# Kernel optimization log

Measured on AMD Instinct MI355X. Metric: run time of the kernel, lower is better.

The kernel has to match this reference:

```python
import jax, jax.numpy as jnp
import numpy as np

jax.config.update("jax_enable_x64", True)

# config
B, S = 4, 4096
H_SIZE = 2048          # hidden_size
VOCAB = 128000         # engram_base_vocab_size
MAX_NGRAM = 3          # engram_max_ngram_size -> orders 2..3
PRIME = 500009         # engram_n_embed_per_ngram (same prime for every order)
N_HEAD = 4             # engram_n_head_per_ngram
E = 32                 # engram_embed_dim
KS = 4                 # short conv kernel size
NUM_ORDERS = MAX_NGRAM - 1
TOTAL_HEADS = NUM_ORDERS * N_HEAD
TOTAL_ROWS = PRIME * N_HEAD * NUM_ORDERS  # flat multi-head table rows


def setup_inputs() -> dict:
    key = jax.random.key(0)
    k_ids, k_h, k_tab, k_cw, k_hp, k_gp, k_op = jax.random.split(key, 7)
    input_ids = jax.random.randint(k_ids, (B, S), 0, VOCAB, dtype=jnp.int64)
    hidden_states = jax.random.normal(k_h, (B, S, H_SIZE), dtype=jnp.float32)
    # identity compressed-tokenizer mapping buffer
    mapping = jnp.arange(VOCAB, dtype=jnp.int64)
    # deterministic odd multipliers, seeded like _build_multipliers
    rng = np.random.default_rng(0 * 10007 + 0 * 1009)
    mults = rng.integers(1, 2 ** 31, size=(NUM_ORDERS, N_HEAD, MAX_NGRAM))
    multipliers = jnp.asarray(mults * 2 + 1, dtype=jnp.int64)
    table = 0.02 * jax.random.normal(k_tab, (TOTAL_ROWS, E), dtype=jnp.float32)
    conv_w = 0.1 * jax.random.normal(k_cw, (E, KS), dtype=jnp.float32)  # depthwise taps
    conv_b = jnp.zeros((E,), dtype=jnp.float32)
    Wh = 0.05 * jax.random.normal(k_hp, (E, TOTAL_HEADS * E), dtype=jnp.float32)
    Wg = 0.02 * jax.random.normal(k_gp, (E, H_SIZE), dtype=jnp.float32)
    Wo = 0.02 * jax.random.normal(k_op, (H_SIZE, E), dtype=jnp.float32)
    return {"input_ids": input_ids, "hidden_states": hidden_states,
            "mapping": mapping, "multipliers": multipliers, "table": table,
            "conv_w": conv_w, "conv_b": conv_b, "Wh": Wh, "Wg": Wg, "Wo": Wo}


def _hash_indices(compressed, multipliers):
    """XOR-mix n-gram hash indices -> [B, S, TOTAL_HEADS] int64."""
    all_idx = []
    offset = 0
    for oi, k in enumerate(range(2, MAX_NGRAM + 1)):
        # forward sliding window, clamped at last token (matches cat/expand trick)
        pos = jnp.minimum(jnp.arange(S)[:, None] + jnp.arange(k)[None, :], S - 1)  # [S,k]
        ng = compressed[:, pos]                                  # [B,S,k]
        m = multipliers[oi, :, :k]                               # [nh,k]
        prod = ng[:, :, None, :] * m[None, None, :, :]           # [B,S,nh,k]
        h = prod[..., 0]
        for p in range(1, k):
            h = h ^ prod[..., p]
        idx = h % PRIME + (offset + jnp.arange(N_HEAD, dtype=jnp.int64) * PRIME)
        all_idx.append(idx)
        offset += PRIME * N_HEAD
    return jnp.concatenate(all_idx, axis=-1)


def reference(input_ids, hidden_states, mapping, multipliers, table,
              conv_w, conv_b, Wh, Wg, Wo):
    compressed = mapping[input_ids]                              # [B,S]
    indices = _hash_indices(compressed, multipliers)             # [B,S,TOTAL_HEADS]
    emb = table[indices].reshape(B, S, TOTAL_HEADS * E)          # multi-head gather
    emb = emb @ Wh.T                                             # head_proj -> [B,S,E]
    # causal depthwise short conv (kernel KS, left pad KS-1)
    xp = jnp.pad(emb, ((0, 0), (KS - 1, 0), (0, 0)))
    emb = sum(xp[:, j:j + S, :] * conv_w[:, j] for j in range(KS)) + conv_b
    gate = jax.nn.sigmoid(hidden_states @ Wg.T)                  # [B,S,E]
    return (gate * emb) @ Wo.T                                   # [B,S,H_SIZE]
```

## Files before the change

kernel.cpp:

```cpp
#include <hip/hip_runtime.h>
#include <hip/hip_bf16.h>
#include <stdint.h>

#define HSZ 2048
#define PRIME 500009u
#define CHUNK 64
#define NCH 32
#define WAVE_REG 16384
#define IDXOFF 65536
#define A_OFF 0
#define E36_OFF 19008
#define GE_OFF 24192

typedef __attribute__((ext_vector_type(8))) short short8;
typedef __attribute__((ext_vector_type(4))) float f32x4;
typedef __attribute__((ext_vector_type(4))) unsigned uint4v;
typedef __attribute__((ext_vector_type(2))) unsigned uint2v;

#define MEMFENCE asm volatile("" ::: "memory")
#define BARRIER() do { MEMFENCE; __builtin_amdgcn_s_barrier(); MEMFENCE; } while (0)
#define WAIT_LGKM0 asm volatile("s_waitcnt lgkmcnt(0)" ::: "memory")
#define WAIT_VM(n) asm volatile("s_waitcnt vmcnt(" #n ")" ::: "memory")

__device__ __forceinline__ unsigned pk2(float x, float y) {
  __hip_bfloat162 h = __float22bfloat162_rn(make_float2(x, y));
  return *reinterpret_cast<unsigned*>(&h);
}
__device__ __forceinline__ short f2bf(float f) {
  __hip_bfloat16 h = __float2bfloat16(f);
  return *reinterpret_cast<short*>(&h);
}
__device__ __forceinline__ short8 pack8(float4 a, float4 b) {
  uint4v u = {pk2(a.x, a.y), pk2(a.z, a.w), pk2(b.x, b.y), pk2(b.z, b.w)};
  return __builtin_bit_cast(short8, u);
}
__device__ __forceinline__ short8 load8_bf(const float* __restrict__ p) {
  float4 a = *reinterpret_cast<const float4*>(p);
  float4 b = *reinterpret_cast<const float4*>(p + 4);
  return pack8(a, b);
}
__device__ __forceinline__ void gload_lds16(const float* g, void* l) {
  __builtin_amdgcn_global_load_lds(
      (const __attribute__((address_space(1))) void*)g,
      (__attribute__((address_space(3))) void*)l, 16, 0, 0);
}

__global__ __launch_bounds__(256, 2) void engram_fused(
    const int* __restrict__ ids, const int* __restrict__ mapping,
    const unsigned* __restrict__ mult, const float* __restrict__ table,
    const float* __restrict__ Wh, const float* __restrict__ hidden,
    const float* __restrict__ cw, const float* __restrict__ cb,
    const float* __restrict__ Wg, const float* __restrict__ Wo,
    float* __restrict__ out) {
  __shared__ __align__(16) char smem[IDXOFF + 1152];
  int* idx_lds = (int*)(smem + IDXOFF);
  short(*A_lds)[264] = (short(*)[264])(smem + A_OFF);
  float(*emb36)[36] = (float(*)[36])(smem + E36_OFF);
  short(*ge_lds)[40] = (short(*)[40])(smem + GE_OFF);

  const int tid = threadIdx.x;
  const int wid = tid >> 6, lane = tid & 63;
  const int l16 = lane & 15, q = lane >> 4;
  const int t0 = blockIdx.x * 32;
  const int tt = wid >> 1, ee = wid & 1;

  char* wavebase = smem + wid * WAVE_REG;

  auto STAGE = [&](int kc) {
    char* hb = wavebase + (kc & 1) * 8192;
#pragma unroll
    for (int j = 0; j < 4; ++j) {
      int r = j * 4 + q;
      unsigned c4 = (((unsigned)l16 * 16u) ^ (((unsigned)r & 7u) << 4)) >> 2;
      gload_lds16(hidden + (size_t)(t0 + tt * 16 + r) * HSZ + kc * CHUNK + c4,
                  hb + j * 1024);
    }
#pragma unroll
    for (int j = 0; j < 4; ++j) {
      int r = j * 4 + q;
      unsigned c4 = (((unsigned)l16 * 16u) ^ (((unsigned)r & 7u) << 4)) >> 2;
      gload_lds16(Wg + (size_t)(ee * 16 + r) * HSZ + kc * CHUNK + c4,
                  hb + 4096 + j * 1024);
    }
  };

#pragma unroll
  for (int p = 0; p < 2; ++p) {
    int hh = p * 256 + tid;
    if (hh < 288) {
      int slot = hh >> 3, head = hh & 7;
      int tg = t0 - 4 + slot;
      if (tg < 0) tg = 0;
      int b = tg >> 12, s = tg & 4095;
      const int* idb = ids + (b << 12);
      int s1 = s + 1 > 4095 ? 4095 : s + 1;
      int s2 = s + 2 > 4095 ? 4095 : s + 2;
      uint64_t c0 = (unsigned)mapping[idb[s]];
      uint64_t c1 = (unsigned)mapping[idb[s1]];
      uint64_t c2 = (unsigned)mapping[idb[s2]];
      int mb = head * 3;
      uint64_t h = (c0 * (uint64_t)mult[mb]) ^ (c1 * (uint64_t)mult[mb + 1]);
      if (head >= 4) h ^= c2 * (uint64_t)mult[mb + 2];
      idx_lds[hh] = (int)((unsigned)(h % PRIME) + (unsigned)head * PRIME);
    }
  }
  WAIT_LGKM0; BARRIER();

  float4 g[9];
#pragma unroll
  for (int p = 0; p < 9; ++p) {
    int task = p * 256 + tid;
    int r = task >> 3, c4 = (task & 7) * 4;
    int row = idx_lds[r];
    g[p] = *reinterpret_cast<const float4*>(table + (size_t)row * 32 + c4);
  }

  STAGE(0);
  STAGE(1);

  const unsigned swz = ((unsigned)l16 & 7u) << 4;
  const char* hrow = wavebase + l16 * 256;
  const char* wrow = wavebase + 4096 + l16 * 256;
  const unsigned x0 = q * 32u;
  f32x4 acc = {0.f, 0.f, 0.f, 0.f};

  auto MLP_ITER = [&](int kc, bool stage_next) {
    const char* hb = hrow + (kc & 1) * 8192;
    const char* wb = wrow + (kc & 1) * 8192;
    float4 a0 = *reinterpret_cast<const float4*>(hb + (x0 ^ swz));
    float4 a1 = *reinterpret_cast<const float4*>(hb + ((x0 + 16) ^ swz));
    float4 a2 = *reinterpret_cast<const float4*>(hb + ((x0 + 128) ^ swz));
    float4 a3 = *reinterpret_cast<const float4*>(hb + ((x0 + 144) ^ swz));
    float4 b0 = *reinterpret_cast<const float4*>(wb + (x0 ^ swz));
    float4 b1 = *reinterpret_cast<const float4*>(wb + ((x0 + 16) ^ swz));
    float4 b2 = *reinterpret_cast<const float4*>(wb + ((x0 + 128) ^ swz));
    float4 b3 = *reinterpret_cast<const float4*>(wb + ((x0 + 144) ^ swz));
    short8 A0 = pack8(a0, a1), A1 = pack8(a2, a3);
    short8 B0 = pack8(b0, b1), B1 = pack8(b2, b3);
    WAIT_LGKM0;
    if (stage_next) STAGE(kc + 2);
    acc = __builtin_amdgcn_mfma_f32_16x16x32_bf16(A0, B0, acc, 0, 0, 0);
    acc = __builtin_amdgcn_mfma_f32_16x16x32_bf16(A1, B1, acc, 0, 0, 0);
  };

  for (int kc = 0; kc < NCH - 1; ++kc) {
    WAIT_VM(8);
    MLP_ITER(kc, kc < NCH - 2);
  }
  { WAIT_VM(0); MLP_ITER(NCH - 1, false); }

  BARRIER();
#pragma unroll
  for (int p = 0; p < 9; ++p) {
    int task = p * 256 + tid;
    int r = task >> 3, c4 = (task & 7) * 4;
    uint2v pk = {pk2(g[p].x, g[p].y), pk2(g[p].z, g[p].w)};
    *reinterpret_cast<uint2v*>(&A_lds[r >> 3][(r & 7) * 32 + c4]) = pk;
  }
  WAIT_LGKM0; BARRIER();

  for (int job = wid; job < 6; job += 4) {
    int jt = job >> 1;
    int base = (jt == 0) ? 0 : (jt == 1) ? 16 : 20;
    int e0 = (job & 1) * 16;
    f32x4 ac = {0.f, 0.f, 0.f, 0.f};
#pragma unroll
    for (int ks = 0; ks < 8; ++ks) {
      short8 wf = load8_bf(Wh + (size_t)(e0 + l16) * 256 + ks * 32 + q * 8);
      short8 a = *reinterpret_cast<const short8*>(&A_lds[base + l16][ks * 32 + q * 8]);
      ac = __builtin_amdgcn_mfma_f32_16x16x32_bf16(wf, a, ac, 0, 0, 0);
    }
    if (jt != 2 || l16 >= 12)
      *reinterpret_cast<f32x4*>(&emb36[base + l16][e0 + q * 4]) = ac;
  }
  WAIT_LGKM0; BARRIER();

  {
    int c = ee * 16 + l16;
    float4 cwv = *reinterpret_cast<const float4*>(cw + c * 4);
    float cbv = cb[c];
#pragma unroll
    for (int j = 0; j < 4; ++j) {
      int r = tt * 16 + q * 4 + j;
      int s = (t0 & 4095) + r;
      float v = cbv;
#pragma unroll
      for (int j2 = 0; j2 < 4; ++j2)
        if (s - 3 + j2 >= 0) v += cwv[j2] * emb36[r + 1 + j2][c];
      float gt = 1.f / (1.f + __expf(-acc[j]));
      ge_lds[r][c] = f2bf(gt * v);
    }
  }
  WAIT_LGKM0; BARRIER();

  short8 Af0 = *reinterpret_cast<const short8*>(&ge_lds[l16][q * 8]);
  short8 Af1 = *reinterpret_cast<const short8*>(&ge_lds[16 + l16][q * 8]);
  float* orow0 = out + (size_t)(t0 + l16) * HSZ;
  float* orow1 = out + (size_t)(t0 + 16 + l16) * HSZ;
  int hbase = wid * 512;
#pragma unroll 4
  for (int ht = 0; ht < 32; ++ht) {
    int h0 = hbase + ht * 16;
    short8 aw = load8_bf(Wo + (size_t)(h0 + l16) * 32 + q * 8);
    f32x4 z = {0.f, 0.f, 0.f, 0.f};
    f32x4 o0 = __builtin_amdgcn_mfma_f32_16x16x32_bf16(aw, Af0, z, 0, 0, 0);
    f32x4 o1 = __builtin_amdgcn_mfma_f32_16x16x32_bf16(aw, Af1, z, 0, 0, 0);
    *reinterpret_cast<f32x4*>(orow0 + h0 + q * 4) = o0;
    *reinterpret_cast<f32x4*>(orow1 + h0 + q * 4) = o1;
  }
}

extern "C" void kernel_launch(void* const* d_in, const int* in_sizes, int n_in,
                              void* d_out, int out_size, void* d_ws, size_t ws_size,
                              hipStream_t stream) {
  const int* ids = (const int*)d_in[0];
  const float* hidden = (const float*)d_in[1];
  const int* mapping = (const int*)d_in[2];
  const unsigned* mult = (const unsigned*)d_in[3];
  const float* table = (const float*)d_in[4];
  const float* cw = (const float*)d_in[5];
  const float* cb = (const float*)d_in[6];
  const float* Wh = (const float*)d_in[7];
  const float* Wg = (const float*)d_in[8];
  const float* Wo = (const float*)d_in[9];
  float* out = (float*)d_out;

  engram_fused<<<512, 256, 0, stream>>>(ids, mapping, mult, table, Wh, hidden,
                                        cw, cb, Wg, Wo, out);
}
```

Baseline: 74.93 us.

## Halve tokens per block and split gate K-reduction across waves

Each block now handles 16 tokens instead of 32, and the four waves split the gate GEMM's K dimension in half (two K-halves by two E-halves), with the partial sums combined through LDS. This halves LDS use per block and doubles the grid to 1024 blocks with launch bounds raised to 4 blocks per SM. The aim is more occupancy and more memory parallelism for the hidden-state streaming. In exchange there is a cross-wave reduction, more halo recomputation of hash and gather per token, and smaller MFMA work per wave in the output projection.

```diff
diff --git a/kernel.cpp b/kernel.cpp
--- a/kernel.cpp
+++ b/kernel.cpp
@@ -4,13 +4,14 @@
 
 #define HSZ 2048
 #define PRIME 500009u
-#define CHUNK 64
+#define CHUNK 32
 #define NCH 32
-#define WAVE_REG 16384
-#define IDXOFF 65536
+#define WAVE_REG 8192
+#define IDXOFF 32768
 #define A_OFF 0
-#define E36_OFF 19008
-#define GE_OFF 24192
+#define E20_OFF 10560
+#define GE_OFF 13440
+#define RED_OFF 14720
 
 typedef __attribute__((ext_vector_type(8))) short short8;
 typedef __attribute__((ext_vector_type(4))) float f32x4;
@@ -45,70 +46,67 @@
       (__attribute__((address_space(3))) void*)l, 16, 0, 0);
 }
 
-__global__ __launch_bounds__(256, 2) void engram_fused(
+__global__ __launch_bounds__(256, 4) void engram_fused(
     const int* __restrict__ ids, const int* __restrict__ mapping,
     const unsigned* __restrict__ mult, const float* __restrict__ table,
     const float* __restrict__ Wh, const float* __restrict__ hidden,
     const float* __restrict__ cw, const float* __restrict__ cb,
     const float* __restrict__ Wg, const float* __restrict__ Wo,
     float* __restrict__ out) {
-  __shared__ __align__(16) char smem[IDXOFF + 1152];
+  __shared__ __align__(16) char smem[IDXOFF + 640];
   int* idx_lds = (int*)(smem + IDXOFF);
   short(*A_lds)[264] = (short(*)[264])(smem + A_OFF);
-  float(*emb36)[36] = (float(*)[36])(smem + E36_OFF);
+  float(*emb20)[36] = (float(*)[36])(smem + E20_OFF);
   short(*ge_lds)[40] = (short(*)[40])(smem + GE_OFF);
+  float(*accred)[4][64] = (float(*)[4][64])(smem + RED_OFF);
 
   const int tid = threadIdx.x;
   const int wid = tid >> 6, lane = tid & 63;
   const int l16 = lane & 15, q = lane >> 4;
-  const int t0 = blockIdx.x * 32;
-  const int tt = wid >> 1, ee = wid & 1;
+  const int t0 = blockIdx.x * 16;
+  const int ee = wid & 1, kh = wid >> 1;
 
   char* wavebase = smem + wid * WAVE_REG;
 
   auto STAGE = [&](int kc) {
-    char* hb = wavebase + (kc & 1) * 8192;
-#pragma unroll
-    for (int j = 0; j < 4; ++j) {
-      int r = j * 4 + q;
-      unsigned c4 = (((unsigned)l16 * 16u) ^ (((unsigned)r & 7u) << 4)) >> 2;
-      gload_lds16(hidden + (size_t)(t0 + tt * 16 + r) * HSZ + kc * CHUNK + c4,
+    char* hb = wavebase + (kc & 1) * 4096;
+#pragma unroll
+    for (int j = 0; j < 2; ++j) {
+      int r = j * 8 + (lane >> 3);
+      unsigned c4 = ((((unsigned)lane & 7u) * 16u) ^ (((unsigned)r & 7u) << 4)) >> 2;
+      gload_lds16(hidden + (size_t)(t0 + r) * HSZ + kh * 1024 + kc * CHUNK + c4,
                   hb + j * 1024);
     }
 #pragma unroll
-    for (int j = 0; j < 4; ++j) {
-      int r = j * 4 + q;
-      unsigned c4 = (((unsigned)l16 * 16u) ^ (((unsigned)r & 7u) << 4)) >> 2;
-      gload_lds16(Wg + (size_t)(ee * 16 + r) * HSZ + kc * CHUNK + c4,
-                  hb + 4096 + j * 1024);
+    for (int j = 0; j < 2; ++j) {
+      int r = j * 8 + (lane >> 3);
+      unsigned c4 = ((((unsigned)lane & 7u) * 16u) ^ (((unsigned)r & 7u) << 4)) >> 2;
+      gload_lds16(Wg + (size_t)(ee * 16 + r) * HSZ + kh * 1024 + kc * CHUNK + c4,
+                  hb + 2048 + j * 1024);
     }
   };
 
-#pragma unroll
-  for (int p = 0; p < 2; ++p) {
-    int hh = p * 256 + tid;
-    if (hh < 288) {
-      int slot = hh >> 3, head = hh & 7;
-      int tg = t0 - 4 + slot;
-      if (tg < 0) tg = 0;
-      int b = tg >> 12, s = tg & 4095;
-      const int* idb = ids + (b << 12);
-      int s1 = s + 1 > 4095 ? 4095 : s + 1;
-      int s2 = s + 2 > 4095 ? 4095 : s + 2;
-      uint64_t c0 = (unsigned)mapping[idb[s]];
-      uint64_t c1 = (unsigned)mapping[idb[s1]];
-      uint64_t c2 = (unsigned)mapping[idb[s2]];
-      int mb = head * 3;
-      uint64_t h = (c0 * (uint64_t)mult[mb]) ^ (c1 * (uint64_t)mult[mb + 1]);
-      if (head >= 4) h ^= c2 * (uint64_t)mult[mb + 2];
-      idx_lds[hh] = (int)((unsigned)(h % PRIME) + (unsigned)head * PRIME);
-    }
-  }
-  WAIT_LGKM0; BARRIER();
-
-  float4 g[9];
-#pragma unroll
-  for (int p = 0; p < 9; ++p) {
+  if (tid < 160) {
+    int slot = tid >> 3, head = tid & 7;
+    int tg = t0 - 4 + slot;
+    if (tg < 0) tg = 0;
+    int b = tg >> 12, s = tg & 4095;
+    const int* idb = ids + (b << 12);
+    int s1 = s + 1 > 4095 ? 4095 : s + 1;
+    int s2 = s + 2 > 4095 ? 4095 : s + 2;
+    uint64_t c0 = (unsigned)mapping[idb[s]];
+    uint64_t c1 = (unsigned)mapping[idb[s1]];
+    uint64_t c2 = (unsigned)mapping[idb[s2]];
+    int mb = head * 3;
+    uint64_t h = (c0 * (uint64_t)mult[mb]) ^ (c1 * (uint64_t)mult[mb + 1]);
+    if (head >= 4) h ^= c2 * (uint64_t)mult[mb + 2];
+    idx_lds[tid] = (int)((unsigned)(h % PRIME) + (unsigned)head * PRIME);
+  }
+  WAIT_LGKM0; BARRIER();
+
+  float4 g[5];
+#pragma unroll
+  for (int p = 0; p < 5; ++p) {
     int task = p * 256 + tid;
     int r = task >> 3, c4 = (task & 7) * 4;
     int row = idx_lds[r];
@@ -119,50 +117,49 @@
   STAGE(1);
 
   const unsigned swz = ((unsigned)l16 & 7u) << 4;
-  const char* hrow = wavebase + l16 * 256;
-  const char* wrow = wavebase + 4096 + l16 * 256;
+  const char* hrow = wavebase + l16 * 128;
+  const char* wrow = wavebase + 2048 + l16 * 128;
   const unsigned x0 = q * 32u;
   f32x4 acc = {0.f, 0.f, 0.f, 0.f};
 
   auto MLP_ITER = [&](int kc, bool stage_next) {
-    const char* hb = hrow + (kc & 1) * 8192;
-    const char* wb = wrow + (kc & 1) * 8192;
+    const char* hb = hrow + (kc & 1) * 4096;
+    const char* wb = wrow + (kc & 1) * 4096;
     float4 a0 = *reinterpret_cast<const float4*>(hb + (x0 ^ swz));
     float4 a1 = *reinterpret_cast<const float4*>(hb + ((x0 + 16) ^ swz));
-    float4 a2 = *reinterpret_cast<const float4*>(hb + ((x0 + 128) ^ swz));
-    float4 a3 = *reinterpret_cast<const float4*>(hb + ((x0 + 144) ^ swz));
     float4 b0 = *reinterpret_cast<const float4*>(wb + (x0 ^ swz));
     float4 b1 = *reinterpret_cast<const float4*>(wb + ((x0 + 16) ^ swz));
-    float4 b2 = *reinterpret_cast<const float4*>(wb + ((x0 + 128) ^ swz));
-    float4 b3 = *reinterpret_cast<const float4*>(wb + ((x0 + 144) ^ swz));
-    short8 A0 = pack8(a0, a1), A1 = pack8(a2, a3);
-    short8 B0 = pack8(b0, b1), B1 = pack8(b2, b3);
+    short8 A0 = pack8(a0, a1);
+    short8 B0 = pack8(b0, b1);
     WAIT_LGKM0;
     if (stage_next) STAGE(kc + 2);
     acc = __builtin_amdgcn_mfma_f32_16x16x32_bf16(A0, B0, acc, 0, 0, 0);
-    acc = __builtin_amdgcn_mfma_f32_16x16x32_bf16(A1, B1, acc, 0, 0, 0);
   };
 
   for (int kc = 0; kc < NCH - 1; ++kc) {
-    WAIT_VM(8);
+    WAIT_VM(4);
     MLP_ITER(kc, kc < NCH - 2);
   }
   { WAIT_VM(0); MLP_ITER(NCH - 1, false); }
 
   BARRIER();
 #pragma unroll
-  for (int p = 0; p < 9; ++p) {
+  for (int p = 0; p < 5; ++p) {
     int task = p * 256 + tid;
     int r = task >> 3, c4 = (task & 7) * 4;
     uint2v pk = {pk2(g[p].x, g[p].y), pk2(g[p].z, g[p].w)};
     *reinterpret_cast<uint2v*>(&A_lds[r >> 3][(r & 7) * 32 + c4]) = pk;
   }
-  WAIT_LGKM0; BARRIER();
-
-  for (int job = wid; job < 6; job += 4) {
-    int jt = job >> 1;
-    int base = (jt == 0) ? 0 : (jt == 1) ? 16 : 20;
-    int e0 = (job & 1) * 16;
+  if (kh == 1) {
+#pragma unroll
+    for (int j = 0; j < 4; ++j) accred[ee][j][lane] = acc[j];
+  }
+  WAIT_LGKM0; BARRIER();
+
+  {
+    int jt = kh;
+    int base = jt ? 4 : 0;
+    int e0 = ee * 16;
     f32x4 ac = {0.f, 0.f, 0.f, 0.f};
 #pragma unroll
     for (int ks = 0; ks < 8; ++ks) {
@@ -170,43 +167,39 @@
       short8 a = *reinterpret_cast<const short8*>(&A_lds[base + l16][ks * 32 + q * 8]);
       ac = __builtin_amdgcn_mfma_f32_16x16x32_bf16(wf, a, ac, 0, 0, 0);
     }
-    if (jt != 2 || l16 >= 12)
-      *reinterpret_cast<f32x4*>(&emb36[base + l16][e0 + q * 4]) = ac;
-  }
-  WAIT_LGKM0; BARRIER();
-
-  {
+    if (jt == 0 || l16 >= 12)
+      *reinterpret_cast<f32x4*>(&emb20[base + l16][e0 + q * 4]) = ac;
+  }
+  WAIT_LGKM0; BARRIER();
+
+  if (kh == 0) {
     int c = ee * 16 + l16;
     float4 cwv = *reinterpret_cast<const float4*>(cw + c * 4);
     float cbv = cb[c];
 #pragma unroll
     for (int j = 0; j < 4; ++j) {
-      int r = tt * 16 + q * 4 + j;
-      int s = (t0 & 4095) + r;
+      int r = q * 4 + j;
+      float s = acc[j] + accred[ee][j][lane];
+      int sp = (t0 & 4095) + r;
       float v = cbv;
 #pragma unroll
       for (int j2 = 0; j2 < 4; ++j2)
-        if (s - 3 + j2 >= 0) v += cwv[j2] * emb36[r + 1 + j2][c];
-      float gt = 1.f / (1.f + __expf(-acc[j]));
+        if (sp - 3 + j2 >= 0) v += cwv[j2] * emb20[r + 1 + j2][c];
+      float gt = 1.f / (1.f + __expf(-s));
       ge_lds[r][c] = f2bf(gt * v);
     }
   }
   WAIT_LGKM0; BARRIER();
 
-  short8 Af0 = *reinterpret_cast<const short8*>(&ge_lds[l16][q * 8]);
-  short8 Af1 = *reinterpret_cast<const short8*>(&ge_lds[16 + l16][q * 8]);
-  float* orow0 = out + (size_t)(t0 + l16) * HSZ;
-  float* orow1 = out + (size_t)(t0 + 16 + l16) * HSZ;
-  int hbase = wid * 512;
+  short8 Af = *reinterpret_cast<const short8*>(&ge_lds[l16][q * 8]);
+  float* orow = out + (size_t)(t0 + l16) * HSZ;
 #pragma unroll 4
   for (int ht = 0; ht < 32; ++ht) {
-    int h0 = hbase + ht * 16;
+    int h0 = wid * 512 + ht * 16;
     short8 aw = load8_bf(Wo + (size_t)(h0 + l16) * 32 + q * 8);
     f32x4 z = {0.f, 0.f, 0.f, 0.f};
-    f32x4 o0 = __builtin_amdgcn_mfma_f32_16x16x32_bf16(aw, Af0, z, 0, 0, 0);
-    f32x4 o1 = __builtin_amdgcn_mfma_f32_16x16x32_bf16(aw, Af1, z, 0, 0, 0);
-    *reinterpret_cast<f32x4*>(orow0 + h0 + q * 4) = o0;
-    *reinterpret_cast<f32x4*>(orow1 + h0 + q * 4) = o1;
+    f32x4 o = __builtin_amdgcn_mfma_f32_16x16x32_bf16(aw, Af, z, 0, 0, 0);
+    *reinterpret_cast<f32x4*>(orow + h0 + q * 4) = o;
   }
 }
 
@@ -225,6 +218,6 @@
   const float* Wo = (const float*)d_in[9];
   float* out = (float*)d_out;
 
-  engram_fused<<<512, 256, 0, stream>>>(ids, mapping, mult, table, Wh, hidden,
-                                        cw, cb, Wg, Wo, out);
-}
+  engram_fused<<<1024, 256, 0, stream>>>(ids, mapping, mult, table, Wh, hidden,
+                                         cw, cb, Wg, Wo, out);
+}
```

Result: slower. 86.81 us (+15.8%).
